# Optimization experiments

Measured on AMD Instinct MI355X. Metric: run time of the kernel, lower is better.

Reference implementation:

```python
import jax, jax.numpy as jnp
import numpy as np

L, H, D, V, CTX = 4, 12, 768, 50257, 2048
HD = D // H
EPS = 1e-5


def setup_inputs() -> dict:
    key = jax.random.key(0)
    ks = jax.random.split(key, 24)
    s = 0.02
    inp = {
        "tokens": jax.random.randint(ks[0], (1, CTX), 0, V, dtype=jnp.int32),
        "vocab_embed": jax.random.normal(ks[1], (V, D), jnp.float32) * s,
        "pos_embed": jax.random.normal(ks[2], (CTX, D), jnp.float32) * s,
        # per-layer stacked params [L, ...]
        "ln1_g": jnp.ones((L, D), jnp.float32),
        "ln1_b": jnp.zeros((L, D), jnp.float32),
        "att_w": jax.random.normal(ks[3], (L, D, 3 * D), jnp.float32) * s,
        "att_b": jnp.zeros((L, 3 * D), jnp.float32),
        "attn_proj_w": jax.random.normal(ks[4], (L, D, D), jnp.float32) * (s / np.sqrt(2 * L)),
        "attn_proj_b": jnp.zeros((L, D), jnp.float32),
        "ln2_g": jnp.ones((L, D), jnp.float32),
        "ln2_b": jnp.zeros((L, D), jnp.float32),
        "fc_w": jax.random.normal(ks[5], (L, D, 4 * D), jnp.float32) * s,
        "fc_b": jnp.zeros((L, 4 * D), jnp.float32),
        "mlp_proj_w": jax.random.normal(ks[6], (L, 4 * D, D), jnp.float32) * (s / np.sqrt(2 * L)),
        "mlp_proj_b": jnp.zeros((L, D), jnp.float32),
        "lnf_g": jnp.ones((D,), jnp.float32),
        "lnf_b": jnp.zeros((D,), jnp.float32),
        "out_w": jax.random.normal(ks[7], (D, V), jnp.float32) * s,
        "out_b": jnp.zeros((V,), jnp.float32),
    }
    return inp


def _layernorm(x, g, b):
    mu = jnp.mean(x, axis=-1, keepdims=True)
    var = jnp.mean(jnp.square(x - mu), axis=-1, keepdims=True)
    return (x - mu) * jax.lax.rsqrt(var + EPS) * g + b


def _gelu(x):
    # exact tanh-approx GELU as in the torch module
    c = np.sqrt(2.0 / np.pi).astype(np.float32)
    return x * 0.5 * (1.0 + jnp.tanh(c * (x + 0.044715 * x * x * x)))


def _forward(tokens, p):
    B, C = tokens.shape
    x = p["vocab_embed"][tokens] + p["pos_embed"][:C][None]  # [B,C,D]
    causal = jnp.tril(jnp.ones((C, C), bool))  # [C,C]
    scale = 1.0 / np.sqrt(HD)
    for l in range(L):
        h = _layernorm(x, p["ln1_g"][l], p["ln1_b"][l])
        qkv = h @ p["att_w"][l] + p["att_b"][l]
        q, k, v = jnp.split(qkv, 3, axis=-1)
        q = q.reshape(B, C, H, HD)
        k = k.reshape(B, C, H, HD)
        v = v.reshape(B, C, H, HD)
        att = jnp.einsum("bqhd,bkhd->bhqk", q, k) * scale
        att = jnp.where(causal[None, None], att, -jnp.inf)
        att = jax.nn.softmax(att, axis=-1)
        o = jnp.einsum("bhqk,bkhd->bqhd", att, v).reshape(B, C, D)
        x = h + (o @ p["attn_proj_w"][l] + p["attn_proj_b"][l])
        h2 = _layernorm(x, p["ln2_g"][l], p["ln2_b"][l])
        mlp = _gelu(h2 @ p["fc_w"][l] + p["fc_b"][l]) @ p["mlp_proj_w"][l] + p["mlp_proj_b"][l]
        x = h2 + mlp
    x = _layernorm(x, p["lnf_g"], p["lnf_b"])
    return x @ p["out_w"] + p["out_b"]  # [B,C,V]


def reference(tokens, vocab_embed, pos_embed, ln1_g, ln1_b, att_w, att_b,
              attn_proj_w, attn_proj_b, ln2_g, ln2_b, fc_w, fc_b,
              mlp_proj_w, mlp_proj_b, lnf_g, lnf_b, out_w, out_b):
    p = dict(vocab_embed=vocab_embed, pos_embed=pos_embed, ln1_g=ln1_g, ln1_b=ln1_b,
             att_w=att_w, att_b=att_b, attn_proj_w=attn_proj_w, attn_proj_b=attn_proj_b,
             ln2_g=ln2_g, ln2_b=ln2_b, fc_w=fc_w, fc_b=fc_b,
             mlp_proj_w=mlp_proj_w, mlp_proj_b=mlp_proj_b,
             lnf_g=lnf_g, lnf_b=lnf_b, out_w=out_w, out_b=out_b)
    return _forward(tokens, p)
```

## Files before the change

### kernel.cpp

```cpp
#include <hip/hip_runtime.h>
#include <hip/hip_bf16.h>
#include <math.h>

#define LAYERS 4
#define NHEAD  12
#define DMODEL 768
#define HEADD  64
#define NCTX   2048
#define NVOCAB 50257
#define NVPAD  50432
#define D3     (3*DMODEL)
#define D4     (4*DMODEL)

typedef short short8 __attribute__((ext_vector_type(8)));
typedef float f32x4  __attribute__((ext_vector_type(4)));
typedef float f32x4u __attribute__((ext_vector_type(4), aligned(4)));
typedef ushort ushx4 __attribute__((ext_vector_type(4)));

__device__ __forceinline__ float bf2f(ushort u) {
    union { uint i; float f; } c; c.i = ((uint)u) << 16; return c.f;
}
__device__ __forceinline__ ushort f2bf(float f) {
    union { float f; uint i; } c; c.f = f;
    uint i = c.i;
    uint r = (i + 0x7FFFu + ((i >> 16) & 1u)) >> 16;
    return (ushort)r;
}

#define GLD16(gp, lp) __builtin_amdgcn_global_load_lds( \
    (__attribute__((address_space(1))) void*)(gp),      \
    (__attribute__((address_space(3))) void*)(lp), 16, 0, 0)

#define BARS() do { asm volatile("s_waitcnt vmcnt(0)" ::: "memory"); \
                    __builtin_amdgcn_s_barrier(); } while (0)

__global__ void embed_k(const int* __restrict__ tok,
                        const float* __restrict__ ve,
                        const float* __restrict__ pe,
                        float* __restrict__ x) {
    int c = blockIdx.x;
    int t = tok[c];
    for (int d = threadIdx.x; d < DMODEL; d += blockDim.x)
        x[(size_t)c * DMODEL + d] = ve[(size_t)t * DMODEL + d] + pe[(size_t)c * DMODEL + d];
}

__global__ __launch_bounds__(256) void ln_v2(const float* __restrict__ x,
                                             const float* __restrict__ g,
                                             const float* __restrict__ b,
                                             float* __restrict__ yf,
                                             ushort* __restrict__ ybf) {
    const int w = threadIdx.x >> 6, l = threadIdx.x & 63;
    const int row = blockIdx.x * 4 + w;
    const float* xr = x + (size_t)row * DMODEL;

    f32x4 v[3];
    float s = 0.f, ss = 0.f;
    #pragma unroll
    for (int i = 0; i < 3; i++) {
        v[i] = *(const f32x4*)(xr + (l + 64 * i) * 4);
        #pragma unroll
        for (int k = 0; k < 4; k++) { s += v[i][k]; ss += v[i][k] * v[i][k]; }
    }
    #pragma unroll
    for (int off = 32; off > 0; off >>= 1) {
        s  += __shfl_xor(s, off);
        ss += __shfl_xor(ss, off);
    }
    const float mu = s * (1.f / DMODEL);
    const float var = ss * (1.f / DMODEL) - mu * mu;
    const float rstd = rsqrtf(var + 1e-5f);

    #pragma unroll
    for (int i = 0; i < 3; i++) {
        const int idx = l + 64 * i;
        f32x4 g4 = *(const f32x4*)(g + idx * 4);
        f32x4 b4 = *(const f32x4*)(b + idx * 4);
        f32x4 r;
        #pragma unroll
        for (int k = 0; k < 4; k++) r[k] = (v[i][k] - mu) * rstd * g4[k] + b4[k];
        if (yf) *(f32x4*)(yf + (size_t)row * DMODEL + idx * 4) = r;
        if (ybf) {
            ushx4 u;
            #pragma unroll
            for (int k = 0; k < 4; k++) u[k] = f2bf(r[k]);
            *(ushx4*)(ybf + (size_t)row * DMODEL + idx * 4) = u;
        }
    }
}

__device__ __forceinline__ void transp64_body(const float* __restrict__ src,
                                              ushort* __restrict__ dst,
                                              int K, int N, int nt, int kt) {
    __shared__ float tile[64][65];
    const int t = threadIdx.x;

    {
        const int r0 = t >> 4;
        const int c  = (t & 15) * 4;
        #pragma unroll
        for (int i = 0; i < 4; i++) {
            const int r = r0 + i * 16;
            const int n = nt + c;
            const float* srow = src + (size_t)(kt + r) * N;
            f32x4 v;
            if (n + 3 < N) {
                v = *(const f32x4u*)(srow + n);
            } else {
                #pragma unroll
                for (int e = 0; e < 4; e++)
                    v[e] = (n + e < N) ? srow[n + e] : 0.f;
            }
            #pragma unroll
            for (int e = 0; e < 4; e++) tile[r][c + e] = v[e];
        }
    }
    __syncthreads();
    {
        const int nl0 = t >> 3;
        const int kb  = (t & 7) * 8;
        #pragma unroll
        for (int h = 0; h < 2; h++) {
            const int nl = nl0 + h * 32;
            short8 o;
            #pragma unroll
            for (int j = 0; j < 8; j++)
                o[j] = (short)f2bf(tile[kb + j][nl]);
            *(short8*)(dst + (size_t)(nt + nl) * K + kt + kb) = o;
        }
    }
}

__global__ __launch_bounds__(256) void transp64(const float* __restrict__ src,
                                                ushort* __restrict__ dst,
                                                int K, int N) {
    transp64_body(src, dst, K, N, blockIdx.x * 64, blockIdx.y * 64);
}

__global__ __launch_bounds__(256) void transp4(
    const float* __restrict__ s0, const float* __restrict__ s1,
    const float* __restrict__ s2, const float* __restrict__ s3,
    ushort* __restrict__ d0, ushort* __restrict__ d1,
    ushort* __restrict__ d2, ushort* __restrict__ d3)
{
    const int bid = blockIdx.x;
    const float* src; ushort* dst; int K, N, nx, tb;
    if (bid < 432)       { src = s0; dst = d0; K = 768;  N = 2304; nx = 36; tb = bid; }
    else if (bid < 576)  { src = s1; dst = d1; K = 768;  N = 768;  nx = 12; tb = bid - 432; }
    else if (bid < 1152) { src = s2; dst = d2; K = 768;  N = 3072; nx = 48; tb = bid - 576; }
    else                 { src = s3; dst = d3; K = 3072; N = 768;  nx = 12; tb = bid - 1152; }
    transp64_body(src, dst, K, N, (tb % nx) * 64, (tb / nx) * 64);
}

template<int MT, int ACT, bool HASADD, bool OUTBF>
__global__ __launch_bounds__(256) void gemm3(
    const ushort* __restrict__ A, const ushort* __restrict__ Bt,
    const float* __restrict__ bias, const ushort* __restrict__ addsrc,
    void* __restrict__ Cout, int N, int K)
{
    constexpr int AFR  = MT / 32;
    constexpr int ABYT = MT * 64;
    constexpr int BUF  = ABYT + 8192;
    constexpr int LPS  = MT / 64 + 2;
    __shared__ __align__(16) char smem[3 * BUF];
    const int bm = blockIdx.y * MT, bn = blockIdx.x * 128;
    const int t = threadIdx.x, l = t & 63, w = t >> 6;
    const int wrb = (w >> 1) * (MT / 2), wcb = (w & 1) * 64;
    const int l15 = l & 15, lg = l >> 4;
    const int swr = ((l15 >> 1) & 3) << 4;

    const int srow = t >> 2;
    const int ssc  = ((t & 3) ^ ((srow >> 1) & 3)) * 8;
    const ushort* Abase = A  + (size_t)(bm + srow) * K + ssc;
    const ushort* Bbase = Bt + (size_t)(bn + srow) * K + ssc;

    f32x4 acc[AFR][4];
    #pragma unroll
    for (int i = 0; i < AFR; i++)
        #pragma unroll
        for (int j = 0; j < 4; j++) acc[i][j] = (f32x4)0.f;

    auto STAGE = [&](int buf, int ke) {
        ushort* as = (ushort*)(smem + buf * BUF);
        ushort* bs = (ushort*)(smem + buf * BUF + ABYT);
        #pragma unroll
        for (int i = 0; i < MT / 64; i++)
            GLD16(Abase + (size_t)i * 64 * K + ke, as + (t + i * 256) * 8);
        #pragma unroll
        for (int i = 0; i < 2; i++)
            GLD16(Bbase + (size_t)i * 64 * K + ke, bs + (t + i * 256) * 8);
    };
    auto COMPUTE = [&](int buf) {
        const char* as = smem + buf * BUF;
        const char* bs = smem + buf * BUF + ABYT;
        short8 af[AFR], bfr[4];
        #pragma unroll
        for (int f = 0; f < AFR; f++)
            af[f] = *(const short8*)(as + (((wrb + f * 16 + l15) * 64 + lg * 16) ^ swr));
        #pragma unroll
        for (int f = 0; f < 4; f++)
            bfr[f] = *(const short8*)(bs + (((wcb + f * 16 + l15) * 64 + lg * 16) ^ swr));
        __builtin_amdgcn_s_setprio(1);
        #pragma unroll
        for (int fm = 0; fm < AFR; fm++)
            #pragma unroll
            for (int fn = 0; fn < 4; fn++)
                acc[fm][fn] = __builtin_amdgcn_mfma_f32_16x16x32_bf16(
                    af[fm], bfr[fn], acc[fm][fn], 0, 0, 0);
        __builtin_amdgcn_s_setprio(0);
    };

    const int nk = K >> 5;
    STAGE(0, 0);
    STAGE(1, 32);
    int bc = 0, bs2 = 2;
    for (int kt = 0; kt < nk; kt++) {
        if (kt < nk - 1)
            asm volatile("s_waitcnt vmcnt(%0)" :: "i"(LPS) : "memory");
        else
            asm volatile("s_waitcnt vmcnt(0)" ::: "memory");
        __builtin_amdgcn_s_barrier();
        asm volatile("" ::: "memory");
        if (kt + 2 < nk) STAGE(bs2, (kt + 2) << 5);
        COMPUTE(bc);
        bc  = (bc  == 2) ? 0 : bc  + 1;
        bs2 = (bs2 == 2) ? 0 : bs2 + 1;
    }

    #pragma unroll
    for (int fn = 0; fn < 4; fn++) {
        const int col = bn + wcb + fn * 16 + l15;
        const float bi = bias[col];
        #pragma unroll
        for (int fm = 0; fm < AFR; fm++) {
            #pragma unroll
            for (int j = 0; j < 4; j++) {
                const int row = bm + wrb + fm * 16 + lg * 4 + j;
                float v = acc[fm][fn][j] + bi;
                if (ACT == 1) {
                    float u = 0.7978845608028654f * (v + 0.044715f * v * v * v);
                    v = 0.5f * v * (1.f + tanhf(u));
                }
                if (HASADD) v += bf2f(addsrc[(size_t)row * N + col]);
                if (OUTBF) ((ushort*)Cout)[(size_t)row * N + col] = f2bf(v);
                else       ((float*) Cout)[(size_t)row * N + col] = v;
            }
        }
    }
}

__global__ __launch_bounds__(1024) void gemm_logits(
    const ushort* __restrict__ A, const ushort* __restrict__ Bt,
    const float* __restrict__ bias, float* __restrict__ Cout)
{
    __shared__ __align__(16) char smem[98304];
    float* Cs = (float*)smem;

    const int pid = (blockIdx.x & 7) * 197 + (blockIdx.x >> 3);
    const int np = pid >> 3, mt = pid & 7;
    const int bm = mt * 256, bn = np * 256;
    const int t = threadIdx.x, l = t & 63, w = t >> 6;
    const int wm = w >> 2, wn = w & 3;
    const int l15 = l & 15, lg = l >> 4;
    const int swr = ((l15 >> 1) & 3) << 4;

    const int sr  = t >> 2;
    const int ssc = ((t & 3) ^ ((sr >> 1) & 3)) * 8;
    const ushort* Ab = A  + (size_t)(bm + sr) * DMODEL + ssc;
    const ushort* Bb = Bt + (size_t)(bn + sr) * DMODEL + ssc;

    f32x4 acc[4][4];
    #pragma unroll
    for (int i = 0; i < 4; i++)
        #pragma unroll
        for (int j = 0; j < 4; j++) acc[i][j] = (f32x4)0.f;

    auto STAGE = [&](int buf, int ke) {
        ushort* as = (ushort*)(smem + buf * 32768);
        ushort* bs = (ushort*)(smem + buf * 32768 + 16384);
        GLD16(Ab + ke, as + t * 8);
        GLD16(Bb + ke, bs + t * 8);
    };
    auto COMPUTE = [&](int buf) {
        const char* as = smem + buf * 32768;
        const char* bs = smem + buf * 32768 + 16384;
        short8 bfr[4];
        #pragma unroll
        for (int f = 0; f < 4; f++) {
            const int r = wn * 64 + f * 16 + l15;
            bfr[f] = *(const short8*)(bs + ((r * 64 + lg * 16) ^ swr));
        }
        __builtin_amdgcn_s_setprio(1);
        #pragma unroll
        for (int fm = 0; fm < 4; fm++) {
            const int r = wm * 64 + fm * 16 + l15;
            short8 af = *(const short8*)(as + ((r * 64 + lg * 16) ^ swr));
            #pragma unroll
            for (int fn = 0; fn < 4; fn++)
                acc[fm][fn] = __builtin_amdgcn_mfma_f32_16x16x32_bf16(
                    af, bfr[fn], acc[fm][fn], 0, 0, 0);
        }
        __builtin_amdgcn_s_setprio(0);
    };

    STAGE(0, 0);
    STAGE(1, 32);
    #pragma unroll
    for (int kt = 0; kt < 24; kt++) {
        if (kt <= 22) asm volatile("s_waitcnt vmcnt(2)" ::: "memory");
        else          asm volatile("s_waitcnt vmcnt(0)" ::: "memory");
        __builtin_amdgcn_s_barrier();
        asm volatile("" ::: "memory");
        if (kt + 2 < 24) STAGE((kt + 2) % 3, (kt + 2) * 32);
        COMPUTE(kt % 3);
    }

    #pragma unroll
    for (int p = 0; p < 4; p++) {
        __syncthreads();
        if (wm == p) {
            #pragma unroll
            for (int fm = 0; fm < 4; fm++) {
                #pragma unroll
                for (int fn = 0; fn < 4; fn++) {
                    const int ccol = wn * 64 + fn * 16 + l15;
                    const int gcol = bn + ccol;
                    const float bi = (gcol < NVOCAB) ? bias[gcol] : 0.f;
                    #pragma unroll
                    for (int j = 0; j < 4; j++)
                        Cs[(fm * 16 + lg * 4 + j) * 256 + ccol] = acc[fm][fn][j] + bi;
                }
            }
        }
        __syncthreads();
        const int grow0 = bm + p * 64;
        #pragma unroll
        for (int i = 0; i < 4; i++) {
            const int idx = t + i * 1024;
            const int rr = idx >> 6, ch = idx & 63;
            f32x4 v = *(const f32x4*)(Cs + rr * 256 + ch * 4);
            float* dst = Cout + (size_t)(grow0 + rr) * NVOCAB + bn + ch * 4;
            if (bn + 256 <= NVOCAB) {
                *(f32x4u*)dst = v;
            } else {
                #pragma unroll
                for (int e = 0; e < 4; e++)
                    if (bn + ch * 4 + e < NVOCAB) dst[e] = v[e];
            }
        }
    }
}

#define QBLK  64
#define KVBLK 64
__global__ __launch_bounds__(256) void qkv_tiles_k(const ushort* __restrict__ qkv,
                                                   ushort* __restrict__ Kimg,
                                                   ushort* __restrict__ Vimg) {
    __shared__ __align__(16) ushort Vt_l[4096];
    const int h = blockIdx.x;
    const int kt = blockIdx.y;
    const int k0 = kt * KVBLK;
    const int t = threadIdx.x;
    ushort* kd = Kimg + ((size_t)h * (NCTX / KVBLK) + kt) * 4096;
    ushort* vd = Vimg + ((size_t)h * (NCTX / KVBLK) + kt) * 4096;

    #pragma unroll
    for (int i = 0; i < 2; i++) {
        const int c = t + i * 256;
        const int r = c >> 3, cc = c & 7;
        short8 kv8 = *(const short8*)(qkv + (size_t)(k0 + r) * D3 + DMODEL + h * HEADD + cc * 8);
        *(short8*)(kd + (((r * 8 + cc) ^ (r & 7)) * 8)) = kv8;
        short8 vv = *(const short8*)(qkv + (size_t)(k0 + r) * D3 + 2 * DMODEL + h * HEADD + cc * 8);
        #pragma unroll
        for (int j = 0; j < 8; j++) {
            const int d = cc * 8 + j;
            const int addr = (d * 128 + r * 2) ^ ((d & 7) << 4);
            *(ushort*)((char*)Vt_l + addr) = (ushort)vv[j];
        }
    }
    __syncthreads();
    #pragma unroll
    for (int i = 0; i < 2; i++) {
        const int c = t + i * 256;
        *(short8*)(vd + c * 8) = *(const short8*)(Vt_l + c * 8);
    }
}

__device__ __forceinline__ void attn_step(
    const short8 qf[2], f32x4 Of[4], float lpart[4],
    const ushort* Kt, const ushort* Vt, char* pw,
    int k0, int q0, int maskTile, int w, int l15, int lg)
{
    const float scale = 0.125f;
    f32x4 S[4];
    __builtin_amdgcn_s_setprio(1);
    #pragma unroll
    for (int nf = 0; nf < 4; nf++) {
        f32x4 a = (f32x4)0.f;
        #pragma unroll
        for (int s = 0; s < 2; s++) {
            const int r = nf * 16 + l15;
            const int addr = (r * 128 + s * 64 + lg * 16) ^ ((r & 7) << 4);
            short8 kf = *(const short8*)((const char*)Kt + addr);
            a = __builtin_amdgcn_mfma_f32_16x16x32_bf16(qf[s], kf, a, 0, 0, 0);
        }
        S[nf] = a;
    }
    __builtin_amdgcn_s_setprio(0);

    float p[4][4];
    if (maskTile) {
        #pragma unroll
        for (int nf = 0; nf < 4; nf++) {
            const int kvg = k0 + nf * 16 + l15;
            #pragma unroll
            for (int j = 0; j < 4; j++) {
                const int qg = q0 + w * 16 + lg * 4 + j;
                p[nf][j] = (kvg <= qg) ? __expf(S[nf][j] * scale) : 0.f;
            }
        }
    } else {
        #pragma unroll
        for (int nf = 0; nf < 4; nf++)
            #pragma unroll
            for (int j = 0; j < 4; j++)
                p[nf][j] = __expf(S[nf][j] * scale);
    }

    #pragma unroll
    for (int j = 0; j < 4; j++)
        lpart[j] += (p[0][j] + p[1][j]) + (p[2][j] + p[3][j]);

    #pragma unroll
    for (int nf = 0; nf < 4; nf++)
        #pragma unroll
        for (int j = 0; j < 4; j++) {
            const int ql = lg * 4 + j;
            const int addr = (ql * 128 + (nf * 16 + l15) * 2) ^ ((ql & 7) << 4);
            *(ushort*)(pw + addr) = f2bf(p[nf][j]);
        }

    __builtin_amdgcn_s_setprio(1);
    #pragma unroll
    for (int s = 0; s < 2; s++) {
        const int paddr = (l15 * 128 + s * 64 + lg * 16) ^ ((l15 & 7) << 4);
        short8 pf = *(const short8*)(pw + paddr);
        #pragma unroll
        for (int df = 0; df < 4; df++) {
            const int r = df * 16 + l15;
            const int vaddr = (r * 128 + s * 64 + lg * 16) ^ ((r & 7) << 4);
            short8 vf = *(const short8*)((const char*)Vt + vaddr);
            Of[df] = __builtin_amdgcn_mfma_f32_16x16x32_bf16(pf, vf, Of[df], 0, 0, 0);
        }
    }
    __builtin_amdgcn_s_setprio(0);
}

__global__ __launch_bounds__(512) void attn_mfma2(const ushort* __restrict__ qkv,
                                                  const ushort* __restrict__ Kimg,
                                                  const ushort* __restrict__ Vimg,
                                                  ushort* __restrict__ o) {
    const int h   = blockIdx.x;
    const int qaT = blockIdx.y;
    const int qbT = 31 - qaT;
    const int t = threadIdx.x;
    const int w = t >> 6;
    const int strm = w >> 2;
    const int ws = w & 3;
    const int l = t & 63;
    const int l15 = l & 15, lg = l >> 4;

    __shared__ __align__(16) ushort Ks[2][16384];
    __shared__ __align__(16) ushort Vs[2][16384];
    __shared__ __align__(16) ushort Ps[8][1024];

    const int myqT = strm ? qbT : qaT;
    const int q0 = myqT * QBLK;
    const ushort* kbase = Kimg + (size_t)h * (NCTX / KVBLK) * 4096;
    const ushort* vbase = Vimg + (size_t)h * (NCTX / KVBLK) * 4096;
    char* pw = (char*)&Ps[w][0];

    short8 qf[2];
    {
        const int qr = q0 + ws * 16 + l15;
        #pragma unroll
        for (int s = 0; s < 2; s++)
            qf[s] = *(const short8*)(qkv + (size_t)qr * D3 + h * HEADD + s * 32 + lg * 8);
    }

    f32x4 Of[4];
    float lpart[4];
    #pragma unroll
    for (int i = 0; i < 4; i++) {
        Of[i] = (f32x4)0.f;
        lpart[i] = 0.f;
    }

    const int ntiles = qbT + 1;
    const int nsteps = (ntiles + 3) >> 2;

    #pragma unroll
    for (int i = 0; i < 4; i++) {
        GLD16(kbase + (size_t)(t + i * 512) * 8, &Ks[0][(t + i * 512) * 8]);
        GLD16(vbase + (size_t)(t + i * 512) * 8, &Vs[0][(t + i * 512) * 8]);
    }

    for (int st = 0; st < nsteps; st++) {
        const int cur = st & 1;
        __syncthreads();
        if (st + 1 < nsteps) {
            const ushort* kim = kbase + (size_t)(st + 1) * 16384;
            const ushort* vim = vbase + (size_t)(st + 1) * 16384;
            #pragma unroll
            for (int i = 0; i < 4; i++) {
                GLD16(kim + (size_t)(t + i * 512) * 8, &Ks[cur ^ 1][(t + i * 512) * 8]);
                GLD16(vim + (size_t)(t + i * 512) * 8, &Vs[cur ^ 1][(t + i * 512) * 8]);
            }
        }
        #pragma unroll
        for (int sub = 0; sub < 4; sub++) {
            const int kt = st * 4 + sub;
            if (kt < ntiles && kt <= myqT)
                attn_step(qf, Of, lpart,
                          &Ks[cur][sub * 4096], &Vs[cur][sub * 4096], pw,
                          kt * KVBLK, q0, (kt == myqT) ? 1 : 0, ws, l15, lg);
        }
    }

    #pragma unroll
    for (int j = 0; j < 4; j++) {
        float lsum = lpart[j];
        lsum += __shfl_xor(lsum, 1);
        lsum += __shfl_xor(lsum, 2);
        lsum += __shfl_xor(lsum, 4);
        lsum += __shfl_xor(lsum, 8);
        const float inv = 1.f / lsum;
        const int qg = q0 + ws * 16 + lg * 4 + j;
        #pragma unroll
        for (int df = 0; df < 4; df++)
            o[(size_t)qg * DMODEL + h * HEADD + df * 16 + l15] = f2bf(Of[df][j] * inv);
    }
}

__global__ void layernorm_k(const float* __restrict__ x,
                            const float* __restrict__ g,
                            const float* __restrict__ b,
                            float* __restrict__ y) {
    const int row = blockIdx.x;
    const float* xr = x + (size_t)row * DMODEL;
    __shared__ float red[256];
    const int tid = threadIdx.x;
    float s = 0.f;
    for (int d = tid; d < DMODEL; d += 256) s += xr[d];
    red[tid] = s; __syncthreads();
    for (int off = 128; off > 0; off >>= 1) {
        if (tid < off) red[tid] += red[tid + off];
        __syncthreads();
    }
    const float mu = red[0] / DMODEL;
    __syncthreads();
    float v = 0.f;
    for (int d = tid; d < DMODEL; d += 256) { float tv = xr[d] - mu; v += tv * tv; }
    red[tid] = v; __syncthreads();
    for (int off = 128; off > 0; off >>= 1) {
        if (tid < off) red[tid] += red[tid + off];
        __syncthreads();
    }
    const float rstd = rsqrtf(red[0] / DMODEL + 1e-5f);
    for (int d = tid; d < DMODEL; d += 256)
        y[(size_t)row * DMODEL + d] = (xr[d] - mu) * rstd * g[d] + b[d];
}

#define BM 64
#define BN 64
#define BK 16
__global__ __launch_bounds__(256)
void gemm_f32(const float* __restrict__ A, const float* __restrict__ B,
              const float* __restrict__ bias, const float* __restrict__ addsrc,
              float* __restrict__ C, int M, int N, int K, int act) {
    __shared__ float As[BK][BM];
    __shared__ float Bs[BK][BN];
    const int bm = blockIdx.y * BM;
    const int bn = blockIdx.x * BN;
    const int tid = threadIdx.x;
    const int tr = tid >> 4;
    const int tc = tid & 15;
    float acc[4][4] = {};
    for (int k0 = 0; k0 < K; k0 += BK) {
        #pragma unroll
        for (int i = 0; i < 4; i++) {
            int idx = tid + i * 256;
            int row = idx >> 4, col = idx & 15;
            int gm = bm + row;
            float v = 0.f;
            if (gm < M) v = A[(size_t)gm * K + (k0 + col)];
            As[col][row] = v;
        }
        #pragma unroll
        for (int i = 0; i < 4; i++) {
            int idx = tid + i * 256;
            int row = idx >> 6, col = idx & 63;
            int gn = bn + col;
            float v = 0.f;
            if (gn < N) v = B[(size_t)(k0 + row) * N + gn];
            Bs[row][col] = v;
        }
        __syncthreads();
        #pragma unroll
        for (int kk = 0; kk < BK; kk++) {
            float a[4], bb[4];
            #pragma unroll
            for (int i = 0; i < 4; i++) a[i] = As[kk][tr * 4 + i];
            #pragma unroll
            for (int j = 0; j < 4; j++) bb[j] = Bs[kk][tc * 4 + j];
            #pragma unroll
            for (int i = 0; i < 4; i++)
                #pragma unroll
                for (int j = 0; j < 4; j++)
                    acc[i][j] += a[i] * bb[j];
        }
        __syncthreads();
    }
    #pragma unroll
    for (int i = 0; i < 4; i++) {
        int gm = bm + tr * 4 + i;
        if (gm >= M) continue;
        #pragma unroll
        for (int j = 0; j < 4; j++) {
            int gn = bn + tc * 4 + j;
            if (gn >= N) continue;
            float v = acc[i][j] + (bias ? bias[gn] : 0.f);
            if (act == 1) {
                const float cst = 0.7978845608028654f;
                float tt = tanhf(cst * (v + 0.044715f * v * v * v));
                v = 0.5f * v * (1.f + tt);
            }
            if (addsrc) v += addsrc[(size_t)gm * N + gn];
            C[(size_t)gm * N + gn] = v;
        }
    }
}

__global__ __launch_bounds__(256)
void attn_k(const float* __restrict__ qkv, float* __restrict__ o) {
    const int q = blockIdx.x;
    const int h = blockIdx.y;
    const int tid = threadIdx.x;
    __shared__ float qrow[HEADD];
    __shared__ float sc[NCTX];
    __shared__ float red[256];
    __shared__ float part[4][HEADD];
    if (tid < HEADD) qrow[tid] = qkv[(size_t)q * D3 + h * HEADD + tid];
    __syncthreads();
    const float scale = 0.125f;
    float lmax = -1e30f;
    for (int k = tid; k <= q; k += 256) {
        const float* kr = qkv + (size_t)k * D3 + DMODEL + h * HEADD;
        float s = 0.f;
        #pragma unroll
        for (int d = 0; d < HEADD; d++) s += qrow[d] * kr[d];
        s *= scale;
        sc[k] = s;
        lmax = fmaxf(lmax, s);
    }
    red[tid] = lmax; __syncthreads();
    for (int off = 128; off > 0; off >>= 1) {
        if (tid < off) red[tid] = fmaxf(red[tid], red[tid + off]);
        __syncthreads();
    }
    const float m = red[0];
    __syncthreads();
    float lsum = 0.f;
    for (int k = tid; k <= q; k += 256) {
        float p = expf(sc[k] - m);
        sc[k] = p;
        lsum += p;
    }
    red[tid] = lsum; __syncthreads();
    for (int off = 128; off > 0; off >>= 1) {
        if (tid < off) red[tid] += red[tid + off];
        __syncthreads();
    }
    const float inv = 1.f / red[0];
    const int grp = tid >> 6;
    const int d = tid & 63;
    float acc = 0.f;
    for (int k = grp; k <= q; k += 4)
        acc += sc[k] * qkv[(size_t)k * D3 + 2 * DMODEL + h * HEADD + d];
    part[grp][d] = acc;
    __syncthreads();
    if (tid < HEADD) {
        float v = (part[0][tid] + part[1][tid] + part[2][tid] + part[3][tid]) * inv;
        o[(size_t)q * DMODEL + h * HEADD + tid] = v;
    }
}

extern "C" void kernel_launch(void* const* d_in, const int* in_sizes, int n_in,
                              void* d_out, int out_size, void* d_ws, size_t ws_size,
                              hipStream_t stream) {
    const int*   tokens      = (const int*)  d_in[0];
    const float* vocab_embed = (const float*)d_in[1];
    const float* pos_embed   = (const float*)d_in[2];
    const float* ln1_g       = (const float*)d_in[3];
    const float* ln1_b       = (const float*)d_in[4];
    const float* att_w       = (const float*)d_in[5];
    const float* att_b       = (const float*)d_in[6];
    const float* attn_proj_w = (const float*)d_in[7];
    const float* attn_proj_b = (const float*)d_in[8];
    const float* ln2_g       = (const float*)d_in[9];
    const float* ln2_b       = (const float*)d_in[10];
    const float* fc_w        = (const float*)d_in[11];
    const float* fc_b        = (const float*)d_in[12];
    const float* mlp_proj_w  = (const float*)d_in[13];
    const float* mlp_proj_b  = (const float*)d_in[14];
    const float* lnf_g       = (const float*)d_in[15];
    const float* lnf_b       = (const float*)d_in[16];
    const float* out_w       = (const float*)d_in[17];
    const float* out_b       = (const float*)d_in[18];
    float* out = (float*)d_out;

    const int C = NCTX;
    dim3 blk(256);

    char* wp = (char*)d_ws;
    size_t used = 0;
    auto carve = [&](size_t bytes) -> void* {
        bytes = (bytes + 255) & ~(size_t)255;
        void* p = wp + used;
        used += bytes;
        return p;
    };
    float*  x_f    = (float*) carve((size_t)C * DMODEL * 4);
    ushort* h_bf   = (ushort*)carve((size_t)C * DMODEL * 2);
    ushort* qkv_bf = (ushort*)carve((size_t)C * D3 * 2);
    ushort* o_bf   = (ushort*)carve((size_t)C * DMODEL * 2);
    ushort* mid_bf = (ushort*)carve((size_t)C * D4 * 2);
    ushort* wt_a   = (ushort*)carve((size_t)D3 * DMODEL * 2);
    ushort* wt_p   = (ushort*)carve((size_t)DMODEL * DMODEL * 2);
    ushort* wt_f   = (ushort*)carve((size_t)D4 * DMODEL * 2);
    ushort* wt_m   = (ushort*)carve((size_t)DMODEL * D4 * 2);
    ushort* wt_out = (ushort*)carve((size_t)NVPAD * DMODEL * 2);
    ushort* Kimg   = (ushort*)carve((size_t)NHEAD * (C / KVBLK) * 4096 * 2);
    ushort* Vimg   = (ushort*)carve((size_t)NHEAD * (C / KVBLK) * 4096 * 2);

    if (ws_size >= used) {
        transp64<<<dim3(NVPAD / 64, DMODEL / 64), blk, 0, stream>>>(
            out_w, wt_out, DMODEL, NVOCAB);

        embed_k<<<dim3(C), blk, 0, stream>>>(tokens, vocab_embed, pos_embed, x_f);

        for (int l = 0; l < LAYERS; l++) {
            transp4<<<dim3(1728), blk, 0, stream>>>(
                att_w + (size_t)l * DMODEL * D3,
                attn_proj_w + (size_t)l * DMODEL * DMODEL,
                fc_w + (size_t)l * DMODEL * D4,
                mlp_proj_w + (size_t)l * D4 * DMODEL,
                wt_a, wt_p, wt_f, wt_m);

            ln_v2<<<dim3(C / 4), blk, 0, stream>>>(
                x_f, ln1_g + l * DMODEL, ln1_b + l * DMODEL, nullptr, h_bf);

            gemm3<128, 0, false, true><<<dim3(D3 / 128, C / 128), blk, 0, stream>>>(
                h_bf, wt_a, att_b + l * D3, nullptr, qkv_bf, D3, DMODEL);

            qkv_tiles_k<<<dim3(NHEAD, C / KVBLK), blk, 0, stream>>>(qkv_bf, Kimg, Vimg);

            attn_mfma2<<<dim3(NHEAD, 16), dim3(512), 0, stream>>>(qkv_bf, Kimg, Vimg, o_bf);

            gemm3<64, 0, true, false><<<dim3(DMODEL / 128, C / 64), blk, 0, stream>>>(
                o_bf, wt_p, attn_proj_b + l * DMODEL, h_bf, x_f, DMODEL, DMODEL);

            ln_v2<<<dim3(C / 4), blk, 0, stream>>>(
                x_f, ln2_g + l * DMODEL, ln2_b + l * DMODEL, nullptr, h_bf);

            gemm3<128, 1, false, true><<<dim3(D4 / 128, C / 128), blk, 0, stream>>>(
                h_bf, wt_f, fc_b + l * D4, nullptr, mid_bf, D4, DMODEL);

            gemm3<64, 0, true, false><<<dim3(DMODEL / 128, C / 64), blk, 0, stream>>>(
                mid_bf, wt_m, mlp_proj_b + l * DMODEL, h_bf, x_f, DMODEL, D4);
        }

        ln_v2<<<dim3(C / 4), blk, 0, stream>>>(x_f, lnf_g, lnf_b, nullptr, h_bf);

        gemm_logits<<<dim3(1576), dim3(1024), 0, stream>>>(h_bf, wt_out, out_b, out);
        return;
    }

    const size_t n_x   = (size_t)C * DMODEL;
    const size_t n_qkv = (size_t)C * D3;
    const size_t need_bytes = (3 * n_x + n_qkv + (size_t)C * D4) * sizeof(float);

    float *x, *h, *o, *qkv, *mid;
    float* ws = (float*)d_ws;
    if (ws_size >= need_bytes) {
        x = ws; h = x + n_x; o = h + n_x; qkv = o + n_x; mid = qkv + n_qkv;
    } else {
        x = ws; h = x + n_x; o = h + n_x;
        qkv = (float*)d_out; mid = qkv + n_qkv;
    }

    embed_k<<<dim3(C), blk, 0, stream>>>(tokens, vocab_embed, pos_embed, x);
    for (int l = 0; l < LAYERS; l++) {
        const float* lw;
        layernorm_k<<<dim3(C), blk, 0, stream>>>(x, ln1_g + l * DMODEL, ln1_b + l * DMODEL, h);
        lw = att_w + (size_t)l * DMODEL * D3;
        gemm_f32<<<dim3(D3 / BN, C / BM), blk, 0, stream>>>(
            h, lw, att_b + l * D3, nullptr, qkv, C, D3, DMODEL, 0);
        attn_k<<<dim3(C, NHEAD), blk, 0, stream>>>(qkv, o);
        lw = attn_proj_w + (size_t)l * DMODEL * DMODEL;
        gemm_f32<<<dim3(DMODEL / BN, C / BM), blk, 0, stream>>>(
            o, lw, attn_proj_b + l * DMODEL, h, x, C, DMODEL, DMODEL, 0);
        layernorm_k<<<dim3(C), blk, 0, stream>>>(x, ln2_g + l * DMODEL, ln2_b + l * DMODEL, h);
        lw = fc_w + (size_t)l * DMODEL * D4;
        gemm_f32<<<dim3(D4 / BN, C / BM), blk, 0, stream>>>(
            h, lw, fc_b + l * D4, nullptr, mid, C, D4, DMODEL, 1);
        lw = mlp_proj_w + (size_t)l * D4 * DMODEL;
        gemm_f32<<<dim3(DMODEL / BN, C / BM), blk, 0, stream>>>(
            mid, lw, mlp_proj_b + l * DMODEL, h, x, C, DMODEL, D4, 0);
    }
    layernorm_k<<<dim3(C), blk, 0, stream>>>(x, lnf_g, lnf_b, h);
    gemm_f32<<<dim3((NVOCAB + BN - 1) / BN, C / BM), blk, 0, stream>>>(
        h, out_w, out_b, nullptr, out, C, NVOCAB, DMODEL, 0);
}
```

Before: 872.6 us.

## Split KV tiles across two wave groups per query tile and double attention grid

Each attention block now processes one query tile instead of a balanced pair. Its two 4-wave groups take alternating KV sub-tiles and merge partial outputs and row sums through shared memory before normalizing. The grid doubles to 32 blocks per head so more CUs get work. In exchange there is uneven per-block work, an extra LDS reduction, and duplicated K/V loads per block.

```diff
diff --git a/kernel.cpp b/kernel.cpp
--- a/kernel.cpp
+++ b/kernel.cpp
@@ -460,8 +460,7 @@
                                                   const ushort* __restrict__ Vimg,
                                                   ushort* __restrict__ o) {
     const int h   = blockIdx.x;
-    const int qaT = blockIdx.y;
-    const int qbT = 31 - qaT;
+    const int myqT = 31 - blockIdx.y;
     const int t = threadIdx.x;
     const int w = t >> 6;
     const int strm = w >> 2;
@@ -473,7 +472,6 @@
     __shared__ __align__(16) ushort Vs[2][16384];
     __shared__ __align__(16) ushort Ps[8][1024];
 
-    const int myqT = strm ? qbT : qaT;
     const int q0 = myqT * QBLK;
     const ushort* kbase = Kimg + (size_t)h * (NCTX / KVBLK) * 4096;
     const ushort* vbase = Vimg + (size_t)h * (NCTX / KVBLK) * 4096;
@@ -495,7 +493,7 @@
         lpart[i] = 0.f;
     }
 
-    const int ntiles = qbT + 1;
+    const int ntiles = myqT + 1;
     const int nsteps = (ntiles + 3) >> 2;
 
     #pragma unroll
@@ -517,27 +515,53 @@
             }
         }
         #pragma unroll
-        for (int sub = 0; sub < 4; sub++) {
+        for (int sub2 = 0; sub2 < 2; sub2++) {
+            const int sub = sub2 * 2 + strm;
             const int kt = st * 4 + sub;
-            if (kt < ntiles && kt <= myqT)
+            if (kt < ntiles)
                 attn_step(qf, Of, lpart,
                           &Ks[cur][sub * 4096], &Vs[cur][sub * 4096], pw,
                           kt * KVBLK, q0, (kt == myqT) ? 1 : 0, ws, l15, lg);
         }
     }
 
-    #pragma unroll
-    for (int j = 0; j < 4; j++) {
-        float lsum = lpart[j];
-        lsum += __shfl_xor(lsum, 1);
-        lsum += __shfl_xor(lsum, 2);
-        lsum += __shfl_xor(lsum, 4);
-        lsum += __shfl_xor(lsum, 8);
-        const float inv = 1.f / lsum;
-        const int qg = q0 + ws * 16 + lg * 4 + j;
+    __syncthreads();
+    float* scr = (float*)&Ks[0][0];
+    const int sidx = (ws * 64 + l) * 21;
+    if (strm == 1) {
         #pragma unroll
         for (int df = 0; df < 4; df++)
-            o[(size_t)qg * DMODEL + h * HEADD + df * 16 + l15] = f2bf(Of[df][j] * inv);
+            #pragma unroll
+            for (int j = 0; j < 4; j++)
+                scr[sidx + df * 4 + j] = Of[df][j];
+        #pragma unroll
+        for (int j = 0; j < 4; j++)
+            scr[sidx + 16 + j] = lpart[j];
+    }
+    __syncthreads();
+    if (strm == 0) {
+        #pragma unroll
+        for (int df = 0; df < 4; df++)
+            #pragma unroll
+            for (int j = 0; j < 4; j++)
+                Of[df][j] += scr[sidx + df * 4 + j];
+        #pragma unroll
+        for (int j = 0; j < 4; j++)
+            lpart[j] += scr[sidx + 16 + j];
+
+        #pragma unroll
+        for (int j = 0; j < 4; j++) {
+            float lsum = lpart[j];
+            lsum += __shfl_xor(lsum, 1);
+            lsum += __shfl_xor(lsum, 2);
+            lsum += __shfl_xor(lsum, 4);
+            lsum += __shfl_xor(lsum, 8);
+            const float inv = 1.f / lsum;
+            const int qg = q0 + ws * 16 + lg * 4 + j;
+            #pragma unroll
+            for (int df = 0; df < 4; df++)
+                o[(size_t)qg * DMODEL + h * HEADD + df * 16 + l15] = f2bf(Of[df][j] * inv);
+        }
     }
 }
 
@@ -764,7 +788,7 @@
 
             qkv_tiles_k<<<dim3(NHEAD, C / KVBLK), blk, 0, stream>>>(qkv_bf, Kimg, Vimg);
 
-            attn_mfma2<<<dim3(NHEAD, 16), dim3(512), 0, stream>>>(qkv_bf, Kimg, Vimg, o_bf);
+            attn_mfma2<<<dim3(NHEAD, 32), dim3(512), 0, stream>>>(qkv_bf, Kimg, Vimg, o_bf);
 
             gemm3<64, 0, true, false><<<dim3(DMODEL / 128, C / 64), blk, 0, stream>>>(
                 o_bf, wt_p, attn_proj_b + l * DMODEL, h_bf, x_f, DMODEL, DMODEL);
```

Measured after the change: 844.1 us. 3.3% less time.
